# Optimization experiments

Hardware: AMD Instinct MI355X
Metric: run time of the kernel (lower is better)

The kernel has to match this reference:

```python
import jax, jax.numpy as jnp
import numpy as np

N_NODES = 50000
N_EDGES = 1000000
D = 66
NEG_SLOPE = 0.2
EPS_BN = 1e-5


def _glorot(key, shape):
    fan = sum(shape)
    lim = jnp.sqrt(6.0 / fan)
    return jax.random.uniform(key, shape, jnp.float32, -lim, lim)


def setup_inputs() -> dict:
    key = jax.random.key(0)
    ks = jax.random.split(key, 40)
    inp = {
        'h': jax.random.normal(ks[0], (N_NODES, D), jnp.float32),
        'edge_index': jax.random.randint(ks[1], (2, N_EDGES), 0, N_NODES, jnp.int32),
        'edge_weight': jax.random.uniform(ks[2], (N_EDGES, 1), jnp.float32),
        'bn_gamma': jnp.ones((D,), jnp.float32),
        'bn_beta': jnp.zeros((D,), jnp.float32),
    }
    i = 3
    for l in (1, 2, 3):
        inp[f'W{l}'] = _glorot(ks[i], (D, D)); i += 1
        inp[f'b{l}'] = jnp.zeros((D,), jnp.float32)
        inp[f'att_src{l}'] = _glorot(ks[i], (D,)); i += 1
        inp[f'att_dst{l}'] = _glorot(ks[i], (D,)); i += 1
        inp[f'We{l}'] = _glorot(ks[i], (1, D)); i += 1
        inp[f'att_e{l}'] = _glorot(ks[i], (D,)); i += 1
    dims = [(D, D), (D, D), (D, D), (D, D), (D, 22)]
    for l, (din, dout) in enumerate(dims, start=1):
        inp[f'fc{l}_w'] = _glorot(ks[i], (din, dout)); i += 1
        inp[f'fc{l}_b'] = jnp.zeros((dout,), jnp.float32)
    return inp


def _gat_conv(h, src, dst, edge_weight, W, b, att_src, att_dst, We, att_e):
    x = h @ W                                     # [N, D]
    a_src = x @ att_src                           # [N]
    a_dst = x @ att_dst                           # [N]
    a_e = (edge_weight @ We) @ att_e              # [E]
    alpha = a_src[src] + a_dst[dst] + a_e         # [E]
    alpha = jnp.where(alpha > 0, alpha, NEG_SLOPE * alpha)
    # scatter-softmax over destination nodes
    m = jax.ops.segment_max(alpha, dst, num_segments=N_NODES)
    m = jnp.where(jnp.isfinite(m), m, 0.0)
    ex = jnp.exp(alpha - m[dst])
    denom = jax.ops.segment_sum(ex, dst, num_segments=N_NODES)
    coef = ex / (denom[dst] + 1e-16)              # [E]
    out = jax.ops.segment_sum(coef[:, None] * x[src], dst, num_segments=N_NODES)
    return out + b


def reference(h, edge_index, edge_weight, bn_gamma, bn_beta,
              W1, b1, att_src1, att_dst1, We1, att_e1,
              W2, b2, att_src2, att_dst2, We2, att_e2,
              W3, b3, att_src3, att_dst3, We3, att_e3,
              fc1_w, fc1_b, fc2_w, fc2_b, fc3_w, fc3_b,
              fc4_w, fc4_b, fc5_w, fc5_b):
    src, dst = edge_index[0], edge_index[1]
    # BatchNorm1d (training-mode batch statistics, biased variance)
    mean = h.mean(0)
    var = ((h - mean) ** 2).mean(0)
    x = (h - mean) * jax.lax.rsqrt(var + EPS_BN) * bn_gamma + bn_beta
    x = jax.nn.relu(_gat_conv(x, src, dst, edge_weight, W1, b1, att_src1, att_dst1, We1, att_e1))
    x = jax.nn.relu(_gat_conv(x, src, dst, edge_weight, W2, b2, att_src2, att_dst2, We2, att_e2))
    x = jax.nn.relu(_gat_conv(x, src, dst, edge_weight, W3, b3, att_src3, att_dst3, We3, att_e3))
    x = jax.nn.relu(x @ fc1_w + fc1_b)
    x = jax.nn.relu(x @ fc2_w + fc2_b)
    x = jax.nn.relu(x @ fc3_w + fc3_b)
    x = jax.nn.relu(x @ fc4_w + fc4_b)
    return x @ fc5_w + fc5_b
```

## Files before the change

### kernel.cpp

```cpp
#include <hip/hip_runtime.h>
#include <math.h>

#define D 66
#define SP 68
#define NEG_SLOPE 0.2f
#define CAP 6144

typedef short s8v __attribute__((ext_vector_type(8)));
typedef float f4v __attribute__((ext_vector_type(4)));

__device__ __forceinline__ float lrelu(float a){ return a > 0.f ? a : NEG_SLOPE * a; }
__device__ __forceinline__ void fma4(float4& a, float s, const float4& w){
  a.x = fmaf(s, w.x, a.x); a.y = fmaf(s, w.y, a.y);
  a.z = fmaf(s, w.z, a.z); a.w = fmaf(s, w.w, a.w);
}
__device__ __forceinline__ unsigned short bf16r(float f){
  unsigned u = __float_as_uint(f);
  u += 0x7FFFu + ((u >> 16) & 1u);
  return (unsigned short)(u >> 16);
}
__device__ __forceinline__ float bf16f(unsigned short b){
  return __uint_as_float(((unsigned)b) << 16);
}
__device__ __forceinline__ void split8t(const float* p, s8v& a0, s8v& a1, s8v& a2){
  #pragma unroll
  for (int j = 0; j < 8; j++){
    float v = p[j];
    unsigned u0 = __float_as_uint(v) & 0xFFFF0000u;
    float r1 = v - __uint_as_float(u0);
    unsigned u1 = __float_as_uint(r1) & 0xFFFF0000u;
    float r2 = r1 - __uint_as_float(u1);
    unsigned u2 = __float_as_uint(r2);
    a0[j] = (short)(u0 >> 16);
    a1[j] = (short)(u1 >> 16);
    a2[j] = (short)(u2 >> 16);
  }
}
#define MM6(acc, a0, a1, a2, b0v, b1v, b2v)                                \
  acc = __builtin_amdgcn_mfma_f32_16x16x32_bf16(a0, b0v, acc, 0, 0, 0);    \
  acc = __builtin_amdgcn_mfma_f32_16x16x32_bf16(a1, b0v, acc, 0, 0, 0);    \
  acc = __builtin_amdgcn_mfma_f32_16x16x32_bf16(a0, b1v, acc, 0, 0, 0);    \
  acc = __builtin_amdgcn_mfma_f32_16x16x32_bf16(a2, b0v, acc, 0, 0, 0);    \
  acc = __builtin_amdgcn_mfma_f32_16x16x32_bf16(a1, b1v, acc, 0, 0, 0);    \
  acc = __builtin_amdgcn_mfma_f32_16x16x32_bf16(a0, b2v, acc, 0, 0, 0);

__global__ __launch_bounds__(256) void k_stats_hist(const float* __restrict__ h, const int* __restrict__ dst,
                                                    float* __restrict__ sums, int* __restrict__ bhist,
                                                    int n, int E){
  int t = threadIdx.x;
  if (blockIdx.x < 256){
    __shared__ float ls[2 * D];
    if (t < 2 * D) ls[t] = 0.f;
    __syncthreads();
    int rpb = (n + 255) / 256;
    int r0 = blockIdx.x * rpb;
    int r1 = min(n, r0 + rpb);
    if (t < 3 * D){
      int c = t % D, seg = t / D;
      float s1 = 0.f, s2 = 0.f;
      for (int r = r0 + seg; r < r1; r += 3){
        float v = h[(size_t)r * D + c];
        s1 += v; s2 += v * v;
      }
      atomicAdd(&ls[c], s1);
      atomicAdd(&ls[D + c], s2);
    }
    __syncthreads();
    if (t < 2 * D) atomicAdd(&sums[t], ls[t]);
  } else {
    __shared__ int hh[256];
    hh[t] = 0;
    __syncthreads();
    int stride = 256 * 256;
    for (int e = (blockIdx.x - 256) * 256 + t; e < E; e += stride)
      atomicAdd(&hh[dst[e] >> 8], 1);
    __syncthreads();
    if (hh[t]) atomicAdd(&bhist[t], hh[t]);
  }
}

struct PrepArgs {
  const float *sums, *gamma, *beta;
  const float *We[3], *ae[3];
  const float *gw[3];
  const float *fw[5], *fb[5];
  float *misc; short *W0, *W1, *W2; short *F0, *F1, *F2; float *bpack;
  int n;
};

__global__ __launch_bounds__(256) void k_prep(PrepArgs pa){
  int t = threadIdx.x;
  if (blockIdx.x == 0){
    if (t < D){
      float mean = pa.sums[t] / (float)pa.n;
      float var  = pa.sums[D + t] / (float)pa.n - mean * mean;
      float inv  = rsqrtf(var + 1e-5f);
      float sc = pa.gamma[t] * inv;
      pa.misc[t] = sc;
      pa.misc[D + t] = pa.beta[t] - mean * sc;
    } else if (t >= D && t < D + 3){
      int l = t - D;
      float c = 0.f;
      for (int d = 0; d < D; d++) c += pa.We[l][d] * pa.ae[l][d];
      pa.misc[2 * D + l] = c;
    }
  } else if (blockIdx.x <= 12){
    int tid = (blockIdx.x - 1) * 256 + t;
    if (tid >= 3 * 960) return;
    int L = tid & 63;
    int ct = (tid >> 6) % 15;
    int lay = tid / 960;
    const float* w = pa.gw[lay];
    int c = ct / 5, tt = ct % 5;
    int nn = tt * 16 + (L & 15);
    int kb = c * 32 + (L >> 4) * 8;
    #pragma unroll
    for (int j = 0; j < 8; j++){
      int k = kb + j;
      float v = (k < D && nn < D) ? w[k * D + nn] : 0.f;
      unsigned short b0 = bf16r(v);  float f0 = bf16f(b0);
      float r1 = v - f0;
      unsigned short b1 = bf16r(r1); float f1 = bf16f(b1);
      unsigned short b2 = bf16r(r1 - f1);
      pa.W0[tid * 8 + j] = (short)b0;
      pa.W1[tid * 8 + j] = (short)b1;
      pa.W2[tid * 8 + j] = (short)b2;
    }
  } else {
    int tid = (blockIdx.x - 13) * 256 + t;
    if (tid < 5 * 960){
      int L = tid & 63;
      int ct = (tid >> 6) % 15;
      int lay = tid / 960;
      const float* w = pa.fw[lay];
      int ncol = (lay == 4) ? 22 : D;
      int c = ct / 5, tt = ct % 5;
      int nn = tt * 16 + (L & 15);
      int kb = c * 32 + (L >> 4) * 8;
      #pragma unroll
      for (int j = 0; j < 8; j++){
        int k = kb + j;
        float v = (k < D && nn < ncol) ? w[k * ncol + nn] : 0.f;
        unsigned short b0 = bf16r(v);  float f0 = bf16f(b0);
        float r1 = v - f0;
        unsigned short b1 = bf16r(r1); float f1 = bf16f(b1);
        unsigned short b2 = bf16r(r1 - f1);
        pa.F0[tid * 8 + j] = (short)b0;
        pa.F1[tid * 8 + j] = (short)b1;
        pa.F2[tid * 8 + j] = (short)b2;
      }
    } else if (tid < 5 * 960 + 400){
      int i = tid - 5 * 960;
      int lay = i / 80, col = i % 80;
      int ncol = (lay == 4) ? 22 : D;
      pa.bpack[i] = (col < ncol) ? pa.fb[lay][col] : 0.f;
    }
  }
}

__global__ void k_bscan(const int* __restrict__ bhist, int* __restrict__ bbase,
                        int* __restrict__ gcur, int* __restrict__ rowptr, int N, int E){
  __shared__ int sh[256];
  int t = threadIdx.x;
  int v = bhist[t];
  sh[t] = v; __syncthreads();
  for (int o = 1; o < 256; o <<= 1){
    int u = (t >= o) ? sh[t - o] : 0;
    __syncthreads();
    sh[t] += u;
    __syncthreads();
  }
  int ex = sh[t] - v;
  bbase[t] = ex;
  gcur[t] = ex;
  if (t == 255){ bbase[256] = sh[255]; rowptr[N] = E; }
}

#define PCHUNK 4096
__global__ __launch_bounds__(256) void k_part(const int* __restrict__ src, const int* __restrict__ dst,
                                              const float* __restrict__ ew,
                                              int* __restrict__ gcur, int2* __restrict__ tmp, int E){
  __shared__ int hist[256];
  __shared__ int base[256];
  int t = threadIdx.x;
  int e0 = blockIdx.x * PCHUNK;
  int eend = min(E, e0 + PCHUNK);
  hist[t] = 0;
  __syncthreads();
  for (int e = e0 + t; e < eend; e += 256)
    atomicAdd(&hist[dst[e] >> 8], 1);
  __syncthreads();
  if (hist[t] > 0) base[t] = atomicAdd(&gcur[t], hist[t]);
  hist[t] = 0;
  __syncthreads();
  for (int e = e0 + t; e < eend; e += 256){
    int d = dst[e];
    int b = d >> 8;
    int off = atomicAdd(&hist[b], 1);
    tmp[base[b] + off] = make_int2((src[e] & 0xffff) | ((d & 255) << 16), __float_as_int(ew[e]));
  }
}

__global__ __launch_bounds__(256) void k_bsort(const int2* __restrict__ tmp, const int* __restrict__ bbase,
                                               int2* __restrict__ epair, int* __restrict__ rowptr, int N){
  __shared__ int2 ebuf[CAP];
  __shared__ int lcnt[256];
  __shared__ int sc[256];
  __shared__ int lcur[256];
  int b = blockIdx.x, t = threadIdx.x;
  int s0 = bbase[b], s1 = bbase[b + 1];
  int cnt = s1 - s0;
  lcnt[t] = 0;
  __syncthreads();
  for (int j = t; j < cnt; j += 256){
    int2 e = tmp[s0 + j];
    if (j < CAP) ebuf[j] = e;
    atomicAdd(&lcnt[(e.x >> 16) & 255], 1);
  }
  __syncthreads();
  int v = lcnt[t];
  sc[t] = v; __syncthreads();
  for (int o = 1; o < 256; o <<= 1){
    int u = (t >= o) ? sc[t - o] : 0;
    __syncthreads();
    sc[t] += u;
    __syncthreads();
  }
  int ex = sc[t] - v;
  int node = (b << 8) + t;
  if (node < N) rowptr[node] = s0 + ex;
  lcur[t] = ex;
  __syncthreads();
  for (int j = t; j < cnt; j += 256){
    int2 e = (j < CAP) ? ebuf[j] : tmp[s0 + j];
    int i = (e.x >> 16) & 255;
    int p = atomicAdd(&lcur[i], 1);
    epair[s0 + p] = make_int2(e.x & 0xffff, e.y);
  }
}

template<bool BN_IN>
__global__ __launch_bounds__(256) void k_mm(const float* __restrict__ X,
    const short* __restrict__ W0, const short* __restrict__ W1, const short* __restrict__ W2,
    const float* __restrict__ att_s, const float* __restrict__ att_d,
    const float* __restrict__ bn,
    float* __restrict__ Y, float* __restrict__ a_src, float* __restrict__ a_dst, int n){
  const int wv = threadIdx.x >> 6, L = threadIdx.x & 63;
  const int quad = L >> 4, m = L & 15;
  const int row0 = blockIdx.x * 64 + wv * 16;
  const int lrow = min(row0 + m, n - 1);
  f4v acc[5];
  #pragma unroll
  for (int t = 0; t < 5; t++) acc[t] = (f4v){0.f,0.f,0.f,0.f};

  #pragma unroll
  for (int c = 0; c < 3; c++){
    float xv[8];
    if (c < 2){
      if (BN_IN){
        const float* hr = X + (size_t)lrow * D + c * 32 + quad * 8;
        #pragma unroll
        for (int j = 0; j < 8; j += 2){
          float2 hv = *(const float2*)(hr + j);
          int col = c * 32 + quad * 8 + j;
          xv[j]     = hv.x * bn[col]     + bn[D + col];
          xv[j + 1] = hv.y * bn[col + 1] + bn[D + col + 1];
        }
      } else {
        const float* xr = X + (size_t)lrow * SP;
        float4 p0 = *(const float4*)&xr[c * 32 + quad * 8];
        float4 p1 = *(const float4*)&xr[c * 32 + quad * 8 + 4];
        xv[0] = p0.x; xv[1] = p0.y; xv[2] = p0.z; xv[3] = p0.w;
        xv[4] = p1.x; xv[5] = p1.y; xv[6] = p1.z; xv[7] = p1.w;
      }
    } else {
      #pragma unroll
      for (int j = 0; j < 8; j++) xv[j] = 0.f;
      if (quad == 0){
        if (BN_IN){
          float2 hv = *(const float2*)(X + (size_t)lrow * D + 64);
          xv[0] = hv.x * bn[64] + bn[D + 64];
          xv[1] = hv.y * bn[65] + bn[D + 65];
        } else {
          float4 p0 = *(const float4*)&X[(size_t)lrow * SP + 64];
          xv[0] = p0.x; xv[1] = p0.y; xv[2] = p0.z; xv[3] = p0.w;
        }
      }
    }
    s8v a0, a1, a2;
    split8t(xv, a0, a1, a2);
    const short* b0p = W0 + (c * 5) * 512 + L * 8;
    const short* b1p = W1 + (c * 5) * 512 + L * 8;
    const short* b2p = W2 + (c * 5) * 512 + L * 8;
    #pragma unroll
    for (int t = 0; t < 5; t++){
      s8v b0v = *(const s8v*)(b0p + t * 512);
      s8v b1v = *(const s8v*)(b1p + t * 512);
      s8v b2v = *(const s8v*)(b2p + t * 512);
      MM6(acc[t], a0, a1, a2, b0v, b1v, b2v)
    }
  }

  float ps[4] = {0.f,0.f,0.f,0.f}, pd[4] = {0.f,0.f,0.f,0.f};
  #pragma unroll
  for (int t = 0; t < 5; t++){
    int col = t * 16 + m;
    float as_v = 0.f, ad_v = 0.f;
    if (col < D){ as_v = att_s[col]; ad_v = att_d[col]; }
    #pragma unroll
    for (int r = 0; r < 4; r++){
      ps[r] += acc[t][r] * as_v;
      pd[r] += acc[t][r] * ad_v;
    }
  }
  #pragma unroll
  for (int r = 0; r < 4; r++){
    int rw = row0 + quad * 4 + r;
    if (rw < n){
      float* yr = Y + (size_t)rw * SP;
      #pragma unroll
      for (int t = 0; t < 4; t++) yr[t * 16 + m] = acc[t][r];
      if (m < 4) yr[64 + m] = (m < 2) ? acc[4][r] : 0.f;
    }
  }
  #pragma unroll
  for (int o = 1; o <= 8; o <<= 1){
    #pragma unroll
    for (int r = 0; r < 4; r++){
      ps[r] += __shfl_xor(ps[r], o);
      pd[r] += __shfl_xor(pd[r], o);
    }
  }
  if (m == 0){
    #pragma unroll
    for (int r = 0; r < 4; r++){
      int rw = row0 + quad * 4 + r;
      if (rw < n){ a_src[rw] = ps[r]; a_dst[rw] = pd[r]; }
    }
  }
}

#define FST 84
__global__ __launch_bounds__(256) void k_fcmm(const float* __restrict__ X,
    const short* __restrict__ W0, const short* __restrict__ W1, const short* __restrict__ W2,
    const float* __restrict__ bpack, float* __restrict__ out, int n){
  __shared__ __align__(16) float xs[2][16][FST];
  const int wv = threadIdx.x >> 6, L = threadIdx.x & 63;
  const int quad = L >> 4, m = L & 15;
  const int rg = wv >> 1, th = wv & 1;
  const int row0 = blockIdx.x * 32 + rg * 16;
  const int lrow = min(row0 + m, n - 1);
  const float* xr = X + (size_t)lrow * SP;

  for (int l = 0; l < 5; l++){
    const int t0 = (l == 4) ? th : (th ? 3 : 0);
    const int nt = (l == 4) ? 1  : (th ? 2 : 3);
    f4v acc[3];
    #pragma unroll
    for (int t = 0; t < 3; t++) acc[t] = (f4v){0.f,0.f,0.f,0.f};
    #pragma unroll
    for (int c = 0; c < 3; c++){
      float xv[8];
      if (l == 0){
        if (c < 2){
          float4 p0 = *(const float4*)&xr[c * 32 + quad * 8];
          float4 p1 = *(const float4*)&xr[c * 32 + quad * 8 + 4];
          xv[0] = p0.x; xv[1] = p0.y; xv[2] = p0.z; xv[3] = p0.w;
          xv[4] = p1.x; xv[5] = p1.y; xv[6] = p1.z; xv[7] = p1.w;
        } else {
          float4 p0 = make_float4(0.f, 0.f, 0.f, 0.f);
          if (quad == 0) p0 = *(const float4*)&xr[64];
          xv[0] = p0.x; xv[1] = p0.y; xv[2] = p0.z; xv[3] = p0.w;
          xv[4] = 0.f; xv[5] = 0.f; xv[6] = 0.f; xv[7] = 0.f;
        }
      } else {
        if (c == 2 && quad >= 2){
          #pragma unroll
          for (int j = 0; j < 8; j++) xv[j] = 0.f;
        } else {
          float4 p0 = *(const float4*)&xs[rg][m][c * 32 + quad * 8];
          float4 p1 = *(const float4*)&xs[rg][m][c * 32 + quad * 8 + 4];
          xv[0] = p0.x; xv[1] = p0.y; xv[2] = p0.z; xv[3] = p0.w;
          xv[4] = p1.x; xv[5] = p1.y; xv[6] = p1.z; xv[7] = p1.w;
        }
      }
      s8v a0, a1, a2;
      split8t(xv, a0, a1, a2);
      const short* b0p = W0 + ((l * 3 + c) * 5 + t0) * 512 + L * 8;
      const short* b1p = W1 + ((l * 3 + c) * 5 + t0) * 512 + L * 8;
      const short* b2p = W2 + ((l * 3 + c) * 5 + t0) * 512 + L * 8;
      for (int t = 0; t < nt; t++){
        s8v b0v = *(const s8v*)(b0p + t * 512);
        s8v b1v = *(const s8v*)(b1p + t * 512);
        s8v b2v = *(const s8v*)(b2p + t * 512);
        MM6(acc[t], a0, a1, a2, b0v, b1v, b2v)
      }
    }
    if (l < 4){
      __syncthreads();
      for (int t = 0; t < nt; t++){
        int col = (t0 + t) * 16 + m;
        float bv = bpack[l * 80 + col];
        #pragma unroll
        for (int r = 0; r < 4; r++){
          float v = acc[t][r] + bv;
          xs[rg][quad * 4 + r][col] = v > 0.f ? v : 0.f;
        }
      }
      __syncthreads();
    } else {
      int col = t0 * 16 + m;
      #pragma unroll
      for (int r = 0; r < 4; r++){
        int rw = row0 + quad * 4 + r;
        if (col < 22 && rw < n) out[(size_t)rw * 22 + col] = acc[0][r] + bpack[4 * 80 + col];
      }
    }
  }
}

__global__ __launch_bounds__(256) void k_agg(const float* __restrict__ y,
                                             const float* __restrict__ a_src, const float* __restrict__ a_dst,
                                             const int* __restrict__ rowptr, const int2* __restrict__ epair,
                                             const float* __restrict__ misc, int cidx,
                                             const float* __restrict__ bias,
                                             float* __restrict__ xout, int n){
  const int wid  = (int)((blockIdx.x * (size_t)blockDim.x + threadIdx.x) >> 6);
  const int lane = threadIdx.x & 63;
  if (wid >= n) return;
  const int beg = rowptr[wid];
  const int deg = rowptr[wid + 1] - beg;
  const float ce  = misc[2 * D + cidx];
  const float adn = a_dst[wid];
  const int g = lane >> 3, q = lane & 7;

  float4 accA = make_float4(0.f,0.f,0.f,0.f);
  float4 accB = make_float4(0.f,0.f,0.f,0.f);
  float2 tacc = make_float2(0.f,0.f);

  if (deg <= 64){
    int s = 0; float al = -INFINITY;
    bool act = lane < deg;
    if (act){
      int2 ep = epair[beg + lane];
      s = ep.x;
      al = lrelu(a_src[s] + adn + ce * __int_as_float(ep.y));
    }
    float mx = al;
    #pragma unroll
    for (int o = 32; o; o >>= 1) mx = fmaxf(mx, __shfl_xor(mx, o));
    float ex = act ? __expf(al - mx) : 0.f;
    float sum = ex;
    #pragma unroll
    for (int o = 32; o; o >>= 1) sum += __shfl_xor(sum, o);
    float coef = ex * (1.f / (sum + 1e-16f));
    for (int e0 = 0; e0 < deg; e0 += 8){
      int e = e0 + g;
      int   st = __shfl(s, e);
      float ct = __shfl(coef, e);
      if (e < deg){
        const float* row = y + (size_t)st * SP;
        float4 y0 = *(const float4*)&row[4 * q];
        float4 y1 = *(const float4*)&row[32 + 4 * q];
        fma4(accA, ct, y0);
        fma4(accB, ct, y1);
        if (q == 0){
          float2 tv = *(const float2*)&row[64];
          tacc.x += ct * tv.x; tacc.y += ct * tv.y;
        }
      }
    }
  } else {
    float mx = -INFINITY;
    for (int j0 = 0; j0 < deg; j0 += 64){
      int j = j0 + lane;
      if (j < deg){
        int2 ep = epair[beg + j];
        mx = fmaxf(mx, lrelu(a_src[ep.x] + adn + ce * __int_as_float(ep.y)));
      }
    }
    #pragma unroll
    for (int o = 32; o; o >>= 1) mx = fmaxf(mx, __shfl_xor(mx, o));
    float sum = 0.f;
    for (int j0 = 0; j0 < deg; j0 += 64){
      int j = j0 + lane;
      if (j < deg){
        int2 ep = epair[beg + j];
        sum += __expf(lrelu(a_src[ep.x] + adn + ce * __int_as_float(ep.y)) - mx);
      }
    }
    #pragma unroll
    for (int o = 32; o; o >>= 1) sum += __shfl_xor(sum, o);
    float inv = 1.f / (sum + 1e-16f);
    for (int j0 = 0; j0 < deg; j0 += 64){
      int cnt = min(64, deg - j0);
      int s = 0; float ex = 0.f;
      if (lane < cnt){
        int2 ep = epair[beg + j0 + lane];
        s = ep.x;
        ex = __expf(lrelu(a_src[s] + adn + ce * __int_as_float(ep.y)) - mx);
      }
      float coef = ex * inv;
      for (int e0 = 0; e0 < cnt; e0 += 8){
        int e = e0 + g;
        int   st = __shfl(s, e);
        float ct = __shfl(coef, e);
        if (e < cnt){
          const float* row = y + (size_t)st * SP;
          float4 y0 = *(const float4*)&row[4 * q];
          float4 y1 = *(const float4*)&row[32 + 4 * q];
          fma4(accA, ct, y0);
          fma4(accB, ct, y1);
          if (q == 0){
            float2 tv = *(const float2*)&row[64];
            tacc.x += ct * tv.x; tacc.y += ct * tv.y;
          }
        }
      }
    }
  }

  #pragma unroll
  for (int o = 8; o <= 32; o <<= 1){
    accA.x += __shfl_xor(accA.x, o); accA.y += __shfl_xor(accA.y, o);
    accA.z += __shfl_xor(accA.z, o); accA.w += __shfl_xor(accA.w, o);
    accB.x += __shfl_xor(accB.x, o); accB.y += __shfl_xor(accB.y, o);
    accB.z += __shfl_xor(accB.z, o); accB.w += __shfl_xor(accB.w, o);
    tacc.x += __shfl_xor(tacc.x, o); tacc.y += __shfl_xor(tacc.y, o);
  }
  float* orow = xout + (size_t)wid * SP;
  if (lane < 8){
    float4 v;
    v.x = accA.x + bias[4*lane+0]; v.x = v.x > 0.f ? v.x : 0.f;
    v.y = accA.y + bias[4*lane+1]; v.y = v.y > 0.f ? v.y : 0.f;
    v.z = accA.z + bias[4*lane+2]; v.z = v.z > 0.f ? v.z : 0.f;
    v.w = accA.w + bias[4*lane+3]; v.w = v.w > 0.f ? v.w : 0.f;
    *(float4*)&orow[4 * lane] = v;
  } else if (lane < 16){
    int qq = lane - 8;
    float4 v;
    v.x = accB.x + bias[32+4*qq+0]; v.x = v.x > 0.f ? v.x : 0.f;
    v.y = accB.y + bias[32+4*qq+1]; v.y = v.y > 0.f ? v.y : 0.f;
    v.z = accB.z + bias[32+4*qq+2]; v.z = v.z > 0.f ? v.z : 0.f;
    v.w = accB.w + bias[32+4*qq+3]; v.w = v.w > 0.f ? v.w : 0.f;
    *(float4*)&orow[32 + 4 * qq] = v;
  }
  if (lane == 0){
    float4 tv;
    tv.x = tacc.x + bias[64]; tv.x = tv.x > 0.f ? tv.x : 0.f;
    tv.y = tacc.y + bias[65]; tv.y = tv.y > 0.f ? tv.y : 0.f;
    tv.z = 0.f; tv.w = 0.f;
    *(float4*)&orow[64] = tv;
  }
}

extern "C" void kernel_launch(void* const* d_in, const int* in_sizes, int n_in,
                              void* d_out, int out_size, void* d_ws, size_t ws_size,
                              hipStream_t stream){
  const float* h     = (const float*)d_in[0];
  const int*   ei    = (const int*)  d_in[1];
  const float* ew    = (const float*)d_in[2];
  const float* gamma = (const float*)d_in[3];
  const float* beta  = (const float*)d_in[4];
  const float *Wl[3], *bl[3], *asl[3], *adl[3], *Wel[3], *ael[3];
  int idx = 5;
  for (int l = 0; l < 3; l++){
    Wl[l]  = (const float*)d_in[idx++];
    bl[l]  = (const float*)d_in[idx++];
    asl[l] = (const float*)d_in[idx++];
    adl[l] = (const float*)d_in[idx++];
    Wel[l] = (const float*)d_in[idx++];
    ael[l] = (const float*)d_in[idx++];
  }
  const float *fw[5], *fb[5];
  for (int l = 0; l < 5; l++){ fw[l] = (const float*)d_in[idx++]; fb[l] = (const float*)d_in[idx++]; }

  int N = in_sizes[0] / D;
  int E = in_sizes[1] / 2;
  const int* src  = ei;
  const int* dstp = ei + E;

  char* base = (char*)d_ws;
  size_t o = 0;
  auto alloc = [&](size_t b){ size_t r = o; o += (b + 255) & ~(size_t)255; return r; };
  float*  bufA   = (float*)(base + alloc((size_t)N * SP * 4));
  float*  bufB   = (float*)(base + alloc((size_t)N * SP * 4));
  float*  a_src  = (float*)(base + alloc((size_t)N * 4));
  float*  a_dst  = (float*)(base + alloc((size_t)N * 4));
  float*  misc   = (float*)(base + alloc(512 * 4));
  float*  sums   = (float*)(base + alloc(2 * D * 4));
  int*    rowptr = (int*)  (base + alloc((size_t)(N + 1) * 4));
  int*    bhist  = (int*)  (base + alloc(256 * 4));
  int*    bbase  = (int*)  (base + alloc(257 * 4));
  int*    gcur   = (int*)  (base + alloc(256 * 4));
  int2*   epair  = (int2*) (base + alloc((size_t)E * 8));
  short*  W0p    = (short*)(base + alloc(3 * 7680 * 2));
  short*  W1p    = (short*)(base + alloc(3 * 7680 * 2));
  short*  W2p    = (short*)(base + alloc(3 * 7680 * 2));
  short*  FW0p   = (short*)(base + alloc(5 * 7680 * 2));
  short*  FW1p   = (short*)(base + alloc(5 * 7680 * 2));
  short*  FW2p   = (short*)(base + alloc(5 * 7680 * 2));
  float*  bpack  = (float*)(base + alloc(400 * 4));
  int2*   tmp    = (int2*)bufB;

  hipMemsetAsync(sums, 0, 2 * D * 4, stream);
  hipMemsetAsync(bhist, 0, 256 * 4, stream);

  k_stats_hist<<<512, 256, 0, stream>>>(h, dstp, sums, bhist, N, E);

  PrepArgs pa;
  pa.sums = sums; pa.gamma = gamma; pa.beta = beta;
  for (int l = 0; l < 3; l++){ pa.We[l] = Wel[l]; pa.ae[l] = ael[l]; pa.gw[l] = Wl[l]; }
  for (int l = 0; l < 5; l++){ pa.fw[l] = fw[l]; pa.fb[l] = fb[l]; }
  pa.misc = misc; pa.W0 = W0p; pa.W1 = W1p; pa.W2 = W2p;
  pa.F0 = FW0p; pa.F1 = FW1p; pa.F2 = FW2p; pa.bpack = bpack; pa.n = N;
  k_prep<<<34, 256, 0, stream>>>(pa);

  int NB = (N + 255) >> 8;
  k_bscan<<<1, 256, 0, stream>>>(bhist, bbase, gcur, rowptr, N, E);
  k_part<<<(E + PCHUNK - 1) / PCHUNK, 256, 0, stream>>>(src, dstp, ew, gcur, tmp, E);
  k_bsort<<<NB, 256, 0, stream>>>(tmp, bbase, epair, rowptr, N);

  int gb = (N + 63) / 64;
  int ab = (N + 3) / 4;

  k_mm<true ><<<gb, 256, 0, stream>>>(h,    W0p + 0 * 7680, W1p + 0 * 7680, W2p + 0 * 7680,
                                      asl[0], adl[0], misc, bufB, a_src, a_dst, N);
  k_agg<<<ab, 256, 0, stream>>>(bufB, a_src, a_dst, rowptr, epair, misc, 0, bl[0], bufA, N);
  k_mm<false><<<gb, 256, 0, stream>>>(bufA, W0p + 1 * 7680, W1p + 1 * 7680, W2p + 1 * 7680,
                                      asl[1], adl[1], misc, bufB, a_src, a_dst, N);
  k_agg<<<ab, 256, 0, stream>>>(bufB, a_src, a_dst, rowptr, epair, misc, 1, bl[1], bufA, N);
  k_mm<false><<<gb, 256, 0, stream>>>(bufA, W0p + 2 * 7680, W1p + 2 * 7680, W2p + 2 * 7680,
                                      asl[2], adl[2], misc, bufB, a_src, a_dst, N);
  k_agg<<<ab, 256, 0, stream>>>(bufB, a_src, a_dst, rowptr, epair, misc, 2, bl[2], bufA, N);

  int gb2 = (N + 31) / 32;
  k_fcmm<<<gb2, 256, 0, stream>>>(bufA, FW0p, FW1p, FW2p, bpack, (float*)d_out, N);
}
```

Baseline: 440.9 us.

## Use two-term bf16 split in MFMA matmuls and process two nodes per wave in aggregation

The matmul and FC kernels now split fp32 operands into two bf16 terms and issue four MFMAs per tile instead of six, dropping the third weight plane and its loads. The GAT aggregation kernel maps two destination nodes onto each 64-lane wave, one per 32-lane half, which suits the average degree of about 20 and leaves fewer lanes idle. Lowering the split to two terms cuts precision from near-fp32 to roughly 16 mantissa bits, which could matter against tolerance. High-degree nodes now fall back to a three-pass loop driven by the larger degree of the two nodes sharing a wave.

```diff
diff --git a/kernel.cpp b/kernel.cpp
--- a/kernel.cpp
+++ b/kernel.cpp
@@ -22,27 +22,21 @@
 __device__ __forceinline__ float bf16f(unsigned short b){
   return __uint_as_float(((unsigned)b) << 16);
 }
-__device__ __forceinline__ void split8t(const float* p, s8v& a0, s8v& a1, s8v& a2){
+__device__ __forceinline__ void split8d(const float* p, s8v& a0, s8v& a1){
   #pragma unroll
   for (int j = 0; j < 8; j++){
     float v = p[j];
     unsigned u0 = __float_as_uint(v) & 0xFFFF0000u;
     float r1 = v - __uint_as_float(u0);
-    unsigned u1 = __float_as_uint(r1) & 0xFFFF0000u;
-    float r2 = r1 - __uint_as_float(u1);
-    unsigned u2 = __float_as_uint(r2);
     a0[j] = (short)(u0 >> 16);
-    a1[j] = (short)(u1 >> 16);
-    a2[j] = (short)(u2 >> 16);
-  }
-}
-#define MM6(acc, a0, a1, a2, b0v, b1v, b2v)                                \
+    a1[j] = (short)(__float_as_uint(r1) >> 16);
+  }
+}
+#define MM4(acc, a0, a1, b0v, b1v)                                         \
   acc = __builtin_amdgcn_mfma_f32_16x16x32_bf16(a0, b0v, acc, 0, 0, 0);    \
   acc = __builtin_amdgcn_mfma_f32_16x16x32_bf16(a1, b0v, acc, 0, 0, 0);    \
   acc = __builtin_amdgcn_mfma_f32_16x16x32_bf16(a0, b1v, acc, 0, 0, 0);    \
-  acc = __builtin_amdgcn_mfma_f32_16x16x32_bf16(a2, b0v, acc, 0, 0, 0);    \
-  acc = __builtin_amdgcn_mfma_f32_16x16x32_bf16(a1, b1v, acc, 0, 0, 0);    \
-  acc = __builtin_amdgcn_mfma_f32_16x16x32_bf16(a0, b2v, acc, 0, 0, 0);
+  acc = __builtin_amdgcn_mfma_f32_16x16x32_bf16(a1, b1v, acc, 0, 0, 0);
 
 __global__ __launch_bounds__(256) void k_stats_hist(const float* __restrict__ h, const int* __restrict__ dst,
                                                     float* __restrict__ sums, int* __restrict__ bhist,
@@ -84,7 +78,7 @@
   const float *We[3], *ae[3];
   const float *gw[3];
   const float *fw[5], *fb[5];
-  float *misc; short *W0, *W1, *W2; short *F0, *F1, *F2; float *bpack;
+  float *misc; short *W0, *W1; short *F0, *F1; float *bpack;
   int n;
 };
 
@@ -118,13 +112,11 @@
     for (int j = 0; j < 8; j++){
       int k = kb + j;
       float v = (k < D && nn < D) ? w[k * D + nn] : 0.f;
-      unsigned short b0 = bf16r(v);  float f0 = bf16f(b0);
-      float r1 = v - f0;
-      unsigned short b1 = bf16r(r1); float f1 = bf16f(b1);
-      unsigned short b2 = bf16r(r1 - f1);
+      unsigned short b0 = bf16r(v);
+      float r1 = v - bf16f(b0);
+      unsigned short b1 = bf16r(r1);
       pa.W0[tid * 8 + j] = (short)b0;
       pa.W1[tid * 8 + j] = (short)b1;
-      pa.W2[tid * 8 + j] = (short)b2;
     }
   } else {
     int tid = (blockIdx.x - 13) * 256 + t;
@@ -141,13 +133,11 @@
       for (int j = 0; j < 8; j++){
         int k = kb + j;
         float v = (k < D && nn < ncol) ? w[k * ncol + nn] : 0.f;
-        unsigned short b0 = bf16r(v);  float f0 = bf16f(b0);
-        float r1 = v - f0;
-        unsigned short b1 = bf16r(r1); float f1 = bf16f(b1);
-        unsigned short b2 = bf16r(r1 - f1);
+        unsigned short b0 = bf16r(v);
+        float r1 = v - bf16f(b0);
+        unsigned short b1 = bf16r(r1);
         pa.F0[tid * 8 + j] = (short)b0;
         pa.F1[tid * 8 + j] = (short)b1;
-        pa.F2[tid * 8 + j] = (short)b2;
       }
     } else if (tid < 5 * 960 + 400){
       int i = tid - 5 * 960;
@@ -241,7 +231,7 @@
 
 template<bool BN_IN>
 __global__ __launch_bounds__(256) void k_mm(const float* __restrict__ X,
-    const short* __restrict__ W0, const short* __restrict__ W1, const short* __restrict__ W2,
+    const short* __restrict__ W0, const short* __restrict__ W1,
     const float* __restrict__ att_s, const float* __restrict__ att_d,
     const float* __restrict__ bn,
     float* __restrict__ Y, float* __restrict__ a_src, float* __restrict__ a_dst, int n){
@@ -287,17 +277,15 @@
         }
       }
     }
-    s8v a0, a1, a2;
-    split8t(xv, a0, a1, a2);
+    s8v a0, a1;
+    split8d(xv, a0, a1);
     const short* b0p = W0 + (c * 5) * 512 + L * 8;
     const short* b1p = W1 + (c * 5) * 512 + L * 8;
-    const short* b2p = W2 + (c * 5) * 512 + L * 8;
     #pragma unroll
     for (int t = 0; t < 5; t++){
       s8v b0v = *(const s8v*)(b0p + t * 512);
       s8v b1v = *(const s8v*)(b1p + t * 512);
-      s8v b2v = *(const s8v*)(b2p + t * 512);
-      MM6(acc[t], a0, a1, a2, b0v, b1v, b2v)
+      MM4(acc[t], a0, a1, b0v, b1v)
     }
   }
 
@@ -342,7 +330,7 @@
 
 #define FST 84
 __global__ __launch_bounds__(256) void k_fcmm(const float* __restrict__ X,
-    const short* __restrict__ W0, const short* __restrict__ W1, const short* __restrict__ W2,
+    const short* __restrict__ W0, const short* __restrict__ W1,
     const float* __restrict__ bpack, float* __restrict__ out, int n){
   __shared__ __align__(16) float xs[2][16][FST];
   const int wv = threadIdx.x >> 6, L = threadIdx.x & 63;
@@ -384,16 +372,14 @@
           xv[4] = p1.x; xv[5] = p1.y; xv[6] = p1.z; xv[7] = p1.w;
         }
       }
-      s8v a0, a1, a2;
-      split8t(xv, a0, a1, a2);
+      s8v a0, a1;
+      split8d(xv, a0, a1);
       const short* b0p = W0 + ((l * 3 + c) * 5 + t0) * 512 + L * 8;
       const short* b1p = W1 + ((l * 3 + c) * 5 + t0) * 512 + L * 8;
-      const short* b2p = W2 + ((l * 3 + c) * 5 + t0) * 512 + L * 8;
       for (int t = 0; t < nt; t++){
         s8v b0v = *(const s8v*)(b0p + t * 512);
         s8v b1v = *(const s8v*)(b1p + t * 512);
-        s8v b2v = *(const s8v*)(b2p + t * 512);
-        MM6(acc[t], a0, a1, a2, b0v, b1v, b2v)
+        MM4(acc[t], a0, a1, b0v, b1v)
       }
     }
     if (l < 4){
@@ -425,45 +411,74 @@
                                              const float* __restrict__ misc, int cidx,
                                              const float* __restrict__ bias,
                                              float* __restrict__ xout, int n){
-  const int wid  = (int)((blockIdx.x * (size_t)blockDim.x + threadIdx.x) >> 6);
+  const int wave = (int)((blockIdx.x * (size_t)blockDim.x + threadIdx.x) >> 6);
   const int lane = threadIdx.x & 63;
-  if (wid >= n) return;
-  const int beg = rowptr[wid];
-  const int deg = rowptr[wid + 1] - beg;
+  const int half = lane >> 5, l32 = lane & 31;
+  const int node = wave * 2 + half;
+  const bool valid = node < n;
+  const int nd = valid ? node : (n - 1);
+  const int beg = rowptr[nd];
+  const int deg = rowptr[nd + 1] - beg;
   const float ce  = misc[2 * D + cidx];
-  const float adn = a_dst[wid];
-  const int g = lane >> 3, q = lane & 7;
-
+  const float adn = a_dst[nd];
+  const int dmax = max(deg, __shfl_xor(deg, 32));
+
+  float mx = -INFINITY, inv;
+  int s = 0; float coef = 0.f;
+
+  if (dmax <= 32){
+    float al = -INFINITY;
+    if (l32 < deg){
+      int2 ep = epair[beg + l32];
+      s = ep.x;
+      al = lrelu(a_src[s] + adn + ce * __int_as_float(ep.y));
+    }
+    mx = al;
+    #pragma unroll
+    for (int o = 16; o; o >>= 1) mx = fmaxf(mx, __shfl_xor(mx, o));
+    float ex = (l32 < deg) ? __expf(al - mx) : 0.f;
+    float sum = ex;
+    #pragma unroll
+    for (int o = 16; o; o >>= 1) sum += __shfl_xor(sum, o);
+    inv = 1.f / (sum + 1e-16f);
+    coef = ex * inv;
+  } else {
+    for (int j0 = 0; j0 < dmax; j0 += 32){
+      int j = j0 + l32;
+      if (j < deg){
+        int2 ep = epair[beg + j];
+        mx = fmaxf(mx, lrelu(a_src[ep.x] + adn + ce * __int_as_float(ep.y)));
+      }
+    }
+    #pragma unroll
+    for (int o = 16; o; o >>= 1) mx = fmaxf(mx, __shfl_xor(mx, o));
+    float sum = 0.f;
+    for (int j0 = 0; j0 < dmax; j0 += 32){
+      int j = j0 + l32;
+      if (j < deg){
+        int2 ep = epair[beg + j];
+        sum += __expf(lrelu(a_src[ep.x] + adn + ce * __int_as_float(ep.y)) - mx);
+      }
+    }
+    #pragma unroll
+    for (int o = 16; o; o >>= 1) sum += __shfl_xor(sum, o);
+    inv = 1.f / (sum + 1e-16f);
+  }
+
+  const int g = l32 >> 3, q = l32 & 7;
   float4 accA = make_float4(0.f,0.f,0.f,0.f);
   float4 accB = make_float4(0.f,0.f,0.f,0.f);
   float2 tacc = make_float2(0.f,0.f);
 
-  if (deg <= 64){
-    int s = 0; float al = -INFINITY;
-    bool act = lane < deg;
-    if (act){
-      int2 ep = epair[beg + lane];
-      s = ep.x;
-      al = lrelu(a_src[s] + adn + ce * __int_as_float(ep.y));
-    }
-    float mx = al;
-    #pragma unroll
-    for (int o = 32; o; o >>= 1) mx = fmaxf(mx, __shfl_xor(mx, o));
-    float ex = act ? __expf(al - mx) : 0.f;
-    float sum = ex;
-    #pragma unroll
-    for (int o = 32; o; o >>= 1) sum += __shfl_xor(sum, o);
-    float coef = ex * (1.f / (sum + 1e-16f));
-    for (int e0 = 0; e0 < deg; e0 += 8){
+  if (dmax <= 32){
+    for (int e0 = 0; e0 < dmax; e0 += 4){
       int e = e0 + g;
-      int   st = __shfl(s, e);
-      float ct = __shfl(coef, e);
+      int   st = __shfl(s,    (lane & 32) | e);
+      float ct = __shfl(coef, (lane & 32) | e);
       if (e < deg){
         const float* row = y + (size_t)st * SP;
-        float4 y0 = *(const float4*)&row[4 * q];
-        float4 y1 = *(const float4*)&row[32 + 4 * q];
-        fma4(accA, ct, y0);
-        fma4(accB, ct, y1);
+        fma4(accA, ct, *(const float4*)&row[4 * q]);
+        fma4(accB, ct, *(const float4*)&row[32 + 4 * q]);
         if (q == 0){
           float2 tv = *(const float2*)&row[64];
           tacc.x += ct * tv.x; tacc.y += ct * tv.y;
@@ -471,46 +486,23 @@
       }
     }
   } else {
-    float mx = -INFINITY;
-    for (int j0 = 0; j0 < deg; j0 += 64){
-      int j = j0 + lane;
+    for (int j0 = 0; j0 < dmax; j0 += 32){
+      int cs = 0; float cc = 0.f;
+      int j = j0 + l32;
       if (j < deg){
         int2 ep = epair[beg + j];
-        mx = fmaxf(mx, lrelu(a_src[ep.x] + adn + ce * __int_as_float(ep.y)));
-      }
-    }
-    #pragma unroll
-    for (int o = 32; o; o >>= 1) mx = fmaxf(mx, __shfl_xor(mx, o));
-    float sum = 0.f;
-    for (int j0 = 0; j0 < deg; j0 += 64){
-      int j = j0 + lane;
-      if (j < deg){
-        int2 ep = epair[beg + j];
-        sum += __expf(lrelu(a_src[ep.x] + adn + ce * __int_as_float(ep.y)) - mx);
-      }
-    }
-    #pragma unroll
-    for (int o = 32; o; o >>= 1) sum += __shfl_xor(sum, o);
-    float inv = 1.f / (sum + 1e-16f);
-    for (int j0 = 0; j0 < deg; j0 += 64){
-      int cnt = min(64, deg - j0);
-      int s = 0; float ex = 0.f;
-      if (lane < cnt){
-        int2 ep = epair[beg + j0 + lane];
-        s = ep.x;
-        ex = __expf(lrelu(a_src[s] + adn + ce * __int_as_float(ep.y)) - mx);
-      }
-      float coef = ex * inv;
-      for (int e0 = 0; e0 < cnt; e0 += 8){
+        cs = ep.x;
+        cc = __expf(lrelu(a_src[cs] + adn + ce * __int_as_float(ep.y)) - mx) * inv;
+      }
+      int cmax = min(32, dmax - j0);
+      for (int e0 = 0; e0 < cmax; e0 += 4){
         int e = e0 + g;
-        int   st = __shfl(s, e);
-        float ct = __shfl(coef, e);
-        if (e < cnt){
+        int   st = __shfl(cs, (lane & 32) | e);
+        float ct = __shfl(cc, (lane & 32) | e);
+        if (j0 + e < deg){
           const float* row = y + (size_t)st * SP;
-          float4 y0 = *(const float4*)&row[4 * q];
-          float4 y1 = *(const float4*)&row[32 + 4 * q];
-          fma4(accA, ct, y0);
-          fma4(accB, ct, y1);
+          fma4(accA, ct, *(const float4*)&row[4 * q]);
+          fma4(accB, ct, *(const float4*)&row[32 + 4 * q]);
           if (q == 0){
             float2 tv = *(const float2*)&row[64];
             tacc.x += ct * tv.x; tacc.y += ct * tv.y;
@@ -521,36 +513,38 @@
   }
 
   #pragma unroll
-  for (int o = 8; o <= 32; o <<= 1){
+  for (int o = 8; o <= 16; o <<= 1){
     accA.x += __shfl_xor(accA.x, o); accA.y += __shfl_xor(accA.y, o);
     accA.z += __shfl_xor(accA.z, o); accA.w += __shfl_xor(accA.w, o);
     accB.x += __shfl_xor(accB.x, o); accB.y += __shfl_xor(accB.y, o);
     accB.z += __shfl_xor(accB.z, o); accB.w += __shfl_xor(accB.w, o);
     tacc.x += __shfl_xor(tacc.x, o); tacc.y += __shfl_xor(tacc.y, o);
   }
-  float* orow = xout + (size_t)wid * SP;
-  if (lane < 8){
-    float4 v;
-    v.x = accA.x + bias[4*lane+0]; v.x = v.x > 0.f ? v.x : 0.f;
-    v.y = accA.y + bias[4*lane+1]; v.y = v.y > 0.f ? v.y : 0.f;
-    v.z = accA.z + bias[4*lane+2]; v.z = v.z > 0.f ? v.z : 0.f;
-    v.w = accA.w + bias[4*lane+3]; v.w = v.w > 0.f ? v.w : 0.f;
-    *(float4*)&orow[4 * lane] = v;
-  } else if (lane < 16){
-    int qq = lane - 8;
-    float4 v;
-    v.x = accB.x + bias[32+4*qq+0]; v.x = v.x > 0.f ? v.x : 0.f;
-    v.y = accB.y + bias[32+4*qq+1]; v.y = v.y > 0.f ? v.y : 0.f;
-    v.z = accB.z + bias[32+4*qq+2]; v.z = v.z > 0.f ? v.z : 0.f;
-    v.w = accB.w + bias[32+4*qq+3]; v.w = v.w > 0.f ? v.w : 0.f;
-    *(float4*)&orow[32 + 4 * qq] = v;
-  }
-  if (lane == 0){
-    float4 tv;
-    tv.x = tacc.x + bias[64]; tv.x = tv.x > 0.f ? tv.x : 0.f;
-    tv.y = tacc.y + bias[65]; tv.y = tv.y > 0.f ? tv.y : 0.f;
-    tv.z = 0.f; tv.w = 0.f;
-    *(float4*)&orow[64] = tv;
+  if (valid){
+    float* orow = xout + (size_t)node * SP;
+    if (l32 < 8){
+      float4 v;
+      v.x = accA.x + bias[4*l32+0]; v.x = v.x > 0.f ? v.x : 0.f;
+      v.y = accA.y + bias[4*l32+1]; v.y = v.y > 0.f ? v.y : 0.f;
+      v.z = accA.z + bias[4*l32+2]; v.z = v.z > 0.f ? v.z : 0.f;
+      v.w = accA.w + bias[4*l32+3]; v.w = v.w > 0.f ? v.w : 0.f;
+      *(float4*)&orow[4 * l32] = v;
+    } else if (l32 < 16){
+      int qq = l32 - 8;
+      float4 v;
+      v.x = accB.x + bias[32+4*qq+0]; v.x = v.x > 0.f ? v.x : 0.f;
+      v.y = accB.y + bias[32+4*qq+1]; v.y = v.y > 0.f ? v.y : 0.f;
+      v.z = accB.z + bias[32+4*qq+2]; v.z = v.z > 0.f ? v.z : 0.f;
+      v.w = accB.w + bias[32+4*qq+3]; v.w = v.w > 0.f ? v.w : 0.f;
+      *(float4*)&orow[32 + 4 * qq] = v;
+    }
+    if (l32 == 0){
+      float4 tv;
+      tv.x = tacc.x + bias[64]; tv.x = tv.x > 0.f ? tv.x : 0.f;
+      tv.y = tacc.y + bias[65]; tv.y = tv.y > 0.f ? tv.y : 0.f;
+      tv.z = 0.f; tv.w = 0.f;
+      *(float4*)&orow[64] = tv;
+    }
   }
 }
 
@@ -596,10 +590,8 @@
   int2*   epair  = (int2*) (base + alloc((size_t)E * 8));
   short*  W0p    = (short*)(base + alloc(3 * 7680 * 2));
   short*  W1p    = (short*)(base + alloc(3 * 7680 * 2));
-  short*  W2p    = (short*)(base + alloc(3 * 7680 * 2));
   short*  FW0p   = (short*)(base + alloc(5 * 7680 * 2));
   short*  FW1p   = (short*)(base + alloc(5 * 7680 * 2));
-  short*  FW2p   = (short*)(base + alloc(5 * 7680 * 2));
   float*  bpack  = (float*)(base + alloc(400 * 4));
   int2*   tmp    = (int2*)bufB;
 
@@ -612,8 +604,8 @@
   pa.sums = sums; pa.gamma = gamma; pa.beta = beta;
   for (int l = 0; l < 3; l++){ pa.We[l] = Wel[l]; pa.ae[l] = ael[l]; pa.gw[l] = Wl[l]; }
   for (int l = 0; l < 5; l++){ pa.fw[l] = fw[l]; pa.fb[l] = fb[l]; }
-  pa.misc = misc; pa.W0 = W0p; pa.W1 = W1p; pa.W2 = W2p;
-  pa.F0 = FW0p; pa.F1 = FW1p; pa.F2 = FW2p; pa.bpack = bpack; pa.n = N;
+  pa.misc = misc; pa.W0 = W0p; pa.W1 = W1p;
+  pa.F0 = FW0p; pa.F1 = FW1p; pa.bpack = bpack; pa.n = N;
   k_prep<<<34, 256, 0, stream>>>(pa);
 
   int NB = (N + 255) >> 8;
@@ -622,18 +614,18 @@
   k_bsort<<<NB, 256, 0, stream>>>(tmp, bbase, epair, rowptr, N);
 
   int gb = (N + 63) / 64;
-  int ab = (N + 3) / 4;
-
-  k_mm<true ><<<gb, 256, 0, stream>>>(h,    W0p + 0 * 7680, W1p + 0 * 7680, W2p + 0 * 7680,
+  int ab = (N + 7) / 8;
+
+  k_mm<true ><<<gb, 256, 0, stream>>>(h,    W0p + 0 * 7680, W1p + 0 * 7680,
                                       asl[0], adl[0], misc, bufB, a_src, a_dst, N);
   k_agg<<<ab, 256, 0, stream>>>(bufB, a_src, a_dst, rowptr, epair, misc, 0, bl[0], bufA, N);
-  k_mm<false><<<gb, 256, 0, stream>>>(bufA, W0p + 1 * 7680, W1p + 1 * 7680, W2p + 1 * 7680,
+  k_mm<false><<<gb, 256, 0, stream>>>(bufA, W0p + 1 * 7680, W1p + 1 * 7680,
                                       asl[1], adl[1], misc, bufB, a_src, a_dst, N);
   k_agg<<<ab, 256, 0, stream>>>(bufB, a_src, a_dst, rowptr, epair, misc, 1, bl[1], bufA, N);
-  k_mm<false><<<gb, 256, 0, stream>>>(bufA, W0p + 2 * 7680, W1p + 2 * 7680, W2p + 2 * 7680,
+  k_mm<false><<<gb, 256, 0, stream>>>(bufA, W0p + 2 * 7680, W1p + 2 * 7680,
                                       asl[2], adl[2], misc, bufB, a_src, a_dst, N);
   k_agg<<<ab, 256, 0, stream>>>(bufB, a_src, a_dst, rowptr, epair, misc, 2, bl[2], bufA, N);
 
   int gb2 = (N + 31) / 32;
-  k_fcmm<<<gb2, 256, 0, stream>>>(bufA, FW0p, FW1p, FW2p, bpack, (float*)d_out, N);
-}
+  k_fcmm<<<gb2, 256, 0, stream>>>(bufA, FW0p, FW1p, bpack, (float*)d_out, N);
+}
```

After: 420.2 us. 1.05x faster.
